# Performance work log

Measured on AMD Instinct MI355X. Metric: run time of the kernel, lower is better.

Reference implementation:

```python
import jax, jax.numpy as jnp
import numpy as np

N0 = 100000; E0 = 1600000; N1 = 100000; E1 = 1600000; G = 512
F0 = 93; F1 = 43
BN_EPS = 1e-5


def setup_inputs() -> dict:
    key = jax.random.key(0)
    ks = jax.random.split(key, 20)
    p = lambda i, shape: jax.random.normal(ks[i], shape, jnp.float32) * 0.02
    return {
        "x_0": jax.random.normal(ks[0], (N0, F0), jnp.float32),
        "x_1": jax.random.normal(ks[1], (N1, F1), jnp.float32),
        "edge_index_0": jax.random.randint(ks[2], (2, E0), 0, N0, jnp.int32),
        "edge_index_1": jax.random.randint(ks[3], (2, E1), 0, N1, jnp.int32),
        "batch_0": jnp.sort(jax.random.randint(ks[4], (N0,), 0, G, jnp.int32)),
        "batch_1": jnp.sort(jax.random.randint(ks[5], (N1,), 0, G, jnp.int32)),
        "w_c1": p(6, (F0, F0)), "b_c1": jnp.zeros((F0,), jnp.float32),
        "w_c2": p(7, (F0, F0 * 10)), "b_c2": jnp.zeros((F0 * 10,), jnp.float32),
        "w_c3": p(8, (F1, F1)), "b_c3": jnp.zeros((F1,), jnp.float32),
        "w_c4": p(9, (F1, F1 * 10)), "b_c4": jnp.zeros((F1 * 10,), jnp.float32),
        "g0_w1": p(10, (F0 * 10 * 2, 1024)), "g0_b1": jnp.zeros((1024,), jnp.float32),
        "g0_w2": p(11, (1024, 512)), "g0_b2": jnp.zeros((512,), jnp.float32),
        "g0_bn_g": jnp.ones((512,), jnp.float32), "g0_bn_b": jnp.zeros((512,), jnp.float32),
        "g1_w1": p(12, (F1 * 10 * 2, 1024)), "g1_b1": jnp.zeros((1024,), jnp.float32),
        "g1_w2": p(13, (1024, 512)), "g1_b2": jnp.zeros((512,), jnp.float32),
        "g1_bn_g": jnp.ones((512,), jnp.float32), "g1_bn_b": jnp.zeros((512,), jnp.float32),
        "f0_w1": p(14, (512, 256)), "f0_b1": jnp.zeros((256,), jnp.float32),
        "f0_w2": p(15, (256, 2)), "f0_b2": jnp.zeros((2,), jnp.float32),
        "f1_w1": p(16, (512, 256)), "f1_b1": jnp.zeros((256,), jnp.float32),
        "f1_w2": p(17, (256, 2)), "f1_b2": jnp.zeros((2,), jnp.float32),
    }


def gin_conv(x, edge_index, W, b):
    # GINConv(eps=0): nn(x + sum_{j->i} x_j); messages from src=edge_index[0] to dst=edge_index[1]
    agg = jax.ops.segment_sum(x[edge_index[0]], edge_index[1], num_segments=x.shape[0])
    return (x + agg) @ W + b


def pool_mean_max(x, batch):
    cnt = jax.ops.segment_sum(jnp.ones((x.shape[0], 1), x.dtype), batch, num_segments=G)
    mean = jax.ops.segment_sum(x, batch, num_segments=G) / jnp.maximum(cnt, 1.0)
    mx = jax.ops.segment_max(x, batch, num_segments=G)
    mx = jnp.where(cnt > 0, mx, 0.0)
    return jnp.concatenate([mean, mx], axis=1)


def batchnorm(x, g, b):
    m = x.mean(axis=0)
    v = x.var(axis=0)
    return g * (x - m) / jnp.sqrt(v + BN_EPS) + b


def branch(x, ei, batch, w_a, b_a, w_b, b_b, w1, b1, w2, b2, bn_g, bn_b):
    h = jax.nn.relu(gin_conv(x, ei, w_a, b_a))
    h = jax.nn.relu(gin_conv(h, ei, w_b, b_b))
    h = pool_mean_max(h, batch)              # [G, 2*10*F] ; PairNorm(mode='None') is identity
    h = jax.nn.relu(h @ w1 + b1)             # dropout: eval mode (identity)
    h = h @ w2 + b2
    return batchnorm(h, bn_g, bn_b)          # [G, 512]


def reference(x_0, x_1, edge_index_0, edge_index_1, batch_0, batch_1,
              w_c1, b_c1, w_c2, b_c2, w_c3, b_c3, w_c4, b_c4,
              g0_w1, g0_b1, g0_w2, g0_b2, g0_bn_g, g0_bn_b,
              g1_w1, g1_b1, g1_w2, g1_b2, g1_bn_g, g1_bn_b,
              f0_w1, f0_b1, f0_w2, f0_b2, f1_w1, f1_b1, f1_w2, f1_b2):
    x_g_0 = branch(x_0, edge_index_0, batch_0, w_c1, b_c1, w_c2, b_c2,
                   g0_w1, g0_b1, g0_w2, g0_b2, g0_bn_g, g0_bn_b)
    z = jax.nn.relu(x_g_0 @ f0_w1 + f0_b1) @ f0_w2 + f0_b2
    x_g_1 = branch(x_1, edge_index_1, batch_1, w_c3, b_c3, w_c4, b_c4,
                   g1_w1, g1_b1, g1_w2, g1_b2, g1_bn_g, g1_bn_b)
    z1 = jax.nn.relu(x_g_1 @ f1_w1 + f1_b1) @ f1_w2 + f1_b2
    return (z, x_g_0, x_g_1, z1)
```

## Files before the change

### kernel.cpp

```cpp
#include <hip/hip_runtime.h>
#include <hip/hip_bf16.h>

#define N0 100000
#define E0C 1600000
#define N1 100000
#define E1C 1600000
#define GCONST 512
#define F0C 93
#define F1C 43
#define OC0 (F0C * 10)
#define OC1 (F1C * 10)
#define BN_EPS 1e-5f
#define NBKT 391
#define SLAB 6016

typedef __attribute__((ext_vector_type(8))) short short8;
typedef __attribute__((ext_vector_type(4))) float floatx4;

static __device__ __forceinline__ unsigned short f2bf(float f) {
    unsigned u = __float_as_uint(f);
    unsigned r = (u + 0x7FFF + ((u >> 16) & 1)) >> 16;
    return (unsigned short)r;
}
static __device__ __forceinline__ float bf2f(unsigned short u) {
    return __uint_as_float(((unsigned)u) << 16);
}
static __device__ __forceinline__ void split_bf(float v, unsigned short& h, unsigned short& l) {
    h = f2bf(v);
    l = f2bf(v - bf2f(h));
}

__global__ __launch_bounds__(256) void misc_kernel(const int* __restrict__ bat0,
                                                   const int* __restrict__ bat1,
                                                   int* __restrict__ st0,
                                                   int* __restrict__ st1,
                                                   int* __restrict__ bcur2) {
    int bid = blockIdx.x;
    int t = threadIdx.x;
    if (bid < 6) {
        int branch = bid / 3;
        const int* batch = branch ? bat1 : bat0;
        int* starts = branch ? st1 : st0;
        int g = (bid % 3) * 256 + t;
        if (g > GCONST) return;
        if (g == GCONST) { starts[GCONST] = N0; return; }
        int lo = 0, hi = N0;
        while (lo < hi) {
            int mid = (lo + hi) >> 1;
            if (batch[mid] < g) lo = mid + 1; else hi = mid;
        }
        starts[g] = lo;
    } else {
        for (int i = t; i < 1024; i += 256) {
            if (i < NBKT) bcur2[i] = i * SLAB;
            else if (i >= 512 && i < 512 + NBKT) bcur2[i] = (i - 512) * SLAB;
        }
    }
}

__global__ __launch_bounds__(256) void edge_bucket2_kernel(const int* __restrict__ ei0,
                                                           const int* __restrict__ ei1,
                                                           int E, int* __restrict__ bcur2,
                                                           int2* __restrict__ st0,
                                                           int2* __restrict__ st1,
                                                           const float* __restrict__ Wc1,
                                                           const float* __restrict__ Wc2,
                                                           const float* __restrict__ Wc3,
                                                           const float* __restrict__ Wc4,
                                                           unsigned short* __restrict__ Ta0,
                                                           unsigned short* __restrict__ Tb0,
                                                           unsigned short* __restrict__ Ta1,
                                                           unsigned short* __restrict__ Tb1,
                                                           unsigned short* __restrict__ p0h,
                                                           unsigned short* __restrict__ p0l,
                                                           unsigned short* __restrict__ p1h,
                                                           unsigned short* __restrict__ p1l) {
    int bid = blockIdx.x;
    int t = threadIdx.x;
    if (bid < 1564) {
        int branch = bid >= 782;
        int blk = branch ? bid - 782 : bid;
        const int* ei = branch ? ei1 : ei0;
        int* bcur = bcur2 + branch * 512;
        int2* staging = branch ? st1 : st0;
        __shared__ int hist[NBKT];
        __shared__ int gbase[NBKT];
        for (int i = t; i < NBKT; i += 256) hist[i] = 0;
        __syncthreads();
        int base = blk * 2048;
        int srcv[8], dstv[8];
#pragma unroll
        for (int i = 0; i < 8; ++i) {
            int e = base + i * 256 + t;
            if (e < E) { srcv[i] = ei[e]; dstv[i] = ei[E + e]; }
            else dstv[i] = -1;
        }
#pragma unroll
        for (int i = 0; i < 8; ++i)
            if (dstv[i] >= 0) atomicAdd(&hist[dstv[i] >> 8], 1);
        __syncthreads();
        for (int i = t; i < NBKT; i += 256) {
            int c = hist[i];
            gbase[i] = c ? atomicAdd(&bcur[i], c) : 0;
            hist[i] = 0;
        }
        __syncthreads();
#pragma unroll
        for (int i = 0; i < 8; ++i) {
            if (dstv[i] >= 0) {
                int b = dstv[i] >> 8;
                int lofs = atomicAdd(&hist[b], 1);
                staging[gbase[b] + lofs] = make_int2(srcv[i], dstv[i]);
            }
        }
    } else if (bid < 3612) {
        int idx = bid - 1564;
        int cfg = idx >> 9;
        int c = (idx & 511) * 2 + (t >> 7);
        int k = t & 127;
        const float* W; unsigned short* T; int OCr, Fr, KP, RB;
        switch (cfg) {
            case 0:  W = Wc1; T = Ta0; OCr = 93;  Fr = 93; KP = 96; RB = 96;   break;
            case 1:  W = Wc2; T = Tb0; OCr = 930; Fr = 93; KP = 96; RB = 1024; break;
            case 2:  W = Wc3; T = Ta1; OCr = 43;  Fr = 43; KP = 64; RB = 48;   break;
            default: W = Wc4; T = Tb1; OCr = 430; Fr = 43; KP = 64; RB = 512;  break;
        }
        if (c >= RB || k >= KP) return;
        unsigned short v = 0;
        if (c < OCr && k < Fr) v = f2bf(W[(size_t)k * OCr + c]);
        T[(size_t)c * KP + k] = v;
    } else if (bid < 3732) {
        int i = (bid - 3612) * 256 + t;
        if (i >= GCONST * 60) return;
        int g = i / 60, c = 1860 + (i - g * 60);
        p0h[(size_t)g * 1920 + c] = 0;
        p0l[(size_t)g * 1920 + c] = 0;
    } else {
        int i = (bid - 3732) * 256 + t;
        if (i >= GCONST * 36) return;
        int g = i / 36, c = 860 + (i - g * 36);
        p1h[(size_t)g * 896 + c] = 0;
        p1l[(size_t)g * 896 + c] = 0;
    }
}

__global__ __launch_bounds__(512) void bucket_scan2_kernel(const int* __restrict__ bcur2,
                                                           int* __restrict__ bbase2) {
    const int* bcur = bcur2 + blockIdx.x * 512;
    int* bbase = bbase2 + blockIdx.x * 512;
    __shared__ int sh[512];
    int t = threadIdx.x;
    int cnt = (t < NBKT) ? bcur[t] - t * SLAB : 0;
    sh[t] = cnt;
    __syncthreads();
    for (int o = 1; o < 512; o <<= 1) {
        int add = (t >= o) ? sh[t - o] : 0;
        __syncthreads();
        sh[t] += add;
        __syncthreads();
    }
    if (t <= NBKT) bbase[t] = sh[t] - cnt;
}

static __device__ __forceinline__ void csr_build_dev(int b, const int2* __restrict__ staging,
                                                     const int* __restrict__ bcur,
                                                     const int* __restrict__ bbase, int N,
                                                     int* __restrict__ rowptr,
                                                     int* __restrict__ col) {
    __shared__ int h[256];
    __shared__ int sc[256];
    int t = threadIdx.x;
    int sl = b * SLAB;
    int se = bcur[b];
    int go = bbase[b];
    h[t] = 0;
    __syncthreads();
    for (int i = sl + t; i < se; i += 256)
        atomicAdd(&h[staging[i].y & 255], 1);
    __syncthreads();
    int v = h[t];
    sc[t] = v;
    __syncthreads();
    for (int o = 1; o < 256; o <<= 1) {
        int add = (t >= o) ? sc[t - o] : 0;
        __syncthreads();
        sc[t] += add;
        __syncthreads();
    }
    int ex = go + (sc[t] - v);
    int node = (b << 8) + t;
    if (node <= N) rowptr[node] = ex;
    __syncthreads();
    sc[t] = ex;
    __syncthreads();
    for (int i = sl + t; i < se; i += 256) {
        int2 ed = staging[i];
        int pos = atomicAdd(&sc[ed.y & 255], 1);
        col[pos] = ed.x;
    }
}

static __device__ __forceinline__ void wsplit_dev(int k0, int c0,
                                                  const float* __restrict__ W,
                                                  unsigned short* __restrict__ Th,
                                                  unsigned short* __restrict__ Tl,
                                                  int K, int N, int KP) {
    __shared__ float tile[32][33];
    int tx = threadIdx.x & 31, ty = threadIdx.x >> 5;
    for (int r = ty; r < 32; r += 8) {
        int k = k0 + r;
        tile[r][tx] = (k < K) ? W[(size_t)k * N + c0 + tx] : 0.f;
    }
    __syncthreads();
    for (int r = ty; r < 32; r += 8) {
        int c = c0 + r;
        float v = tile[tx][r];
        unsigned short h, l;
        split_bf(v, h, l);
        Th[(size_t)c * KP + k0 + tx] = h;
        Tl[(size_t)c * KP + k0 + tx] = l;
    }
}

template<int KP, int CH, int GR>
static __device__ __forceinline__ void gather_dev(int nb, unsigned short* __restrict__ t,
                                                  const unsigned short* __restrict__ x,
                                                  const int* __restrict__ rowptr,
                                                  const int* __restrict__ col, int N) {
    int wave = threadIdx.x >> 6, lane = threadIdx.x & 63;
    int node = nb * 4 + wave;
    if (node >= N) return;
    int g = lane / CH;
    int c = lane - g * CH;
    bool act = (g < GR);
    int s = rowptr[node], e = rowptr[node + 1];
    float acc[8] = {0.f, 0.f, 0.f, 0.f, 0.f, 0.f, 0.f, 0.f};
    int j = act ? (s - 1 + g) : e;
    int src0 = node;
    if (j >= s && j < e) src0 = col[j];
    while (j < e) {
        int jb = j + GR;
        int jc = jb + GR;
        int srcb = (jb < e) ? col[jb] : 0;
        int srcc = (jc < e) ? col[jc] : 0;
        short8 v0 = *(const short8*)(x + (size_t)src0 * KP + c * 8);
#pragma unroll
        for (int i = 0; i < 8; ++i) acc[i] += bf2f((unsigned short)v0[i]);
        if (jb < e) {
            short8 v1 = *(const short8*)(x + (size_t)srcb * KP + c * 8);
#pragma unroll
            for (int i = 0; i < 8; ++i) acc[i] += bf2f((unsigned short)v1[i]);
        }
        j = jc; src0 = srcc;
    }
    if (GR == 8) {
#pragma unroll
        for (int i = 0; i < 8; ++i) {
            float v = acc[i];
            v += __shfl_xor(v, 8);
            v += __shfl_xor(v, 16);
            v += __shfl_xor(v, 32);
            acc[i] = v;
        }
    } else {
#pragma unroll
        for (int i = 0; i < 8; ++i) {
            float v = acc[i];
            float v1 = __shfl(v, lane + CH);
            float v2 = __shfl(v, lane + 2 * CH);
            float v3 = __shfl(v, lane + 3 * CH);
            float v4 = __shfl(v, lane + 4 * CH);
            acc[i] = v + v1 + v2 + v3 + v4;
        }
    }
    if (lane < CH) {
        short8 o;
#pragma unroll
        for (int i = 0; i < 8; ++i) o[i] = (short)f2bf(acc[i]);
        *(short8*)(t + (size_t)node * KP + lane * 8) = o;
    }
}

template<int KP, int KS, int NT>
static __device__ __forceinline__ void conv1_dev(int nb, const unsigned short* __restrict__ t,
                                                 const unsigned short* __restrict__ Wt,
                                                 const float* __restrict__ bias,
                                                 unsigned short* __restrict__ y,
                                                 int NC, int N) {
    int wave = threadIdx.x >> 6, lane = threadIdx.x & 63;
    int quad = lane >> 4, l15 = lane & 15;
    int r0 = (nb * 4 + wave) * 16;
    const short8 z8 = {0, 0, 0, 0, 0, 0, 0, 0};
    short8 a[KS];
    int arow = r0 + l15;
#pragma unroll
    for (int ks = 0; ks < KS; ++ks)
        a[ks] = (arow < N) ? *(const short8*)(t + (size_t)arow * KP + ks * 32 + quad * 8) : z8;
#pragma unroll
    for (int nt = 0; nt < NT; ++nt) {
        int colb = nt * 16 + l15;
        floatx4 c = {0.f, 0.f, 0.f, 0.f};
#pragma unroll
        for (int ks = 0; ks < KS; ++ks) {
            short8 b = *(const short8*)(Wt + (size_t)colb * KP + ks * 32 + quad * 8);
            c = __builtin_amdgcn_mfma_f32_16x16x32_bf16(a[ks], b, c, 0, 0, 0);
        }
        float bc = (colb < NC) ? bias[colb] : 0.f;
#pragma unroll
        for (int r = 0; r < 4; ++r) {
            int row = r0 + quad * 4 + r;
            if (row < N) {
                float o = fmaxf(c[r] + bc, 0.f);
                y[(size_t)row * KP + colb] = f2bf(o);
            }
        }
    }
}

template<int KP, int KS>
static __device__ __forceinline__ void conv2_pool_dev(int cb, int g,
                                                      const unsigned short* __restrict__ t,
                                                      const unsigned short* __restrict__ Wt,
                                                      const float* __restrict__ bias,
                                                      const int* __restrict__ starts,
                                                      unsigned short* __restrict__ ph,
                                                      unsigned short* __restrict__ pl,
                                                      int OC, int KPad) {
    int wave = threadIdx.x >> 6, lane = threadIdx.x & 63;
    int quad = lane >> 4, l15 = lane & 15;
    int cw0 = cb * 256 + wave * 64;
    short8 bfr[4][KS];
    float bs[4];
#pragma unroll
    for (int ti = 0; ti < 4; ++ti) {
        int colb = cw0 + ti * 16 + l15;
#pragma unroll
        for (int ks = 0; ks < KS; ++ks)
            bfr[ti][ks] = *(const short8*)(Wt + (size_t)colb * KP + ks * 32 + quad * 8);
        bs[ti] = (colb < OC) ? bias[colb] : 0.f;
    }
    int s = starts[g], e = starts[g + 1];
    float sum[4] = {0.f, 0.f, 0.f, 0.f};
    float mx[4]  = {0.f, 0.f, 0.f, 0.f};
    const short8 z8 = {0, 0, 0, 0, 0, 0, 0, 0};
    for (int ns = s; ns < e; ns += 16) {
        short8 a[KS];
        int arow = ns + l15;
        bool av = arow < e;
#pragma unroll
        for (int ks = 0; ks < KS; ++ks)
            a[ks] = av ? *(const short8*)(t + (size_t)arow * KP + ks * 32 + quad * 8) : z8;
        int rbase = ns + quad * 4;
#pragma unroll
        for (int ti = 0; ti < 4; ++ti) {
            floatx4 c = {0.f, 0.f, 0.f, 0.f};
#pragma unroll
            for (int ks = 0; ks < KS; ++ks)
                c = __builtin_amdgcn_mfma_f32_16x16x32_bf16(a[ks], bfr[ti][ks], c, 0, 0, 0);
#pragma unroll
            for (int r = 0; r < 4; ++r) {
                float o = fmaxf(c[r] + bs[ti], 0.f);
                if (rbase + r < e) {
                    sum[ti] += o;
                    mx[ti] = fmaxf(mx[ti], o);
                }
            }
        }
    }
    int cnt = e - s;
    float rc = 1.f / (float)(cnt > 0 ? cnt : 1);
#pragma unroll
    for (int ti = 0; ti < 4; ++ti) {
        float sv = sum[ti], mv = mx[ti];
        sv += __shfl_down(sv, 32);
        mv = fmaxf(mv, __shfl_down(mv, 32));
        sv += __shfl_down(sv, 16);
        mv = fmaxf(mv, __shfl_down(mv, 16));
        if (lane < 16) {
            int colb = cw0 + ti * 16 + l15;
            if (colb < OC) {
                size_t base = (size_t)g * (size_t)KPad;
                unsigned short h, l;
                split_bf(sv * rc, h, l);
                ph[base + colb] = h; pl[base + colb] = l;
                split_bf(mv, h, l);
                ph[base + OC + colb] = h; pl[base + OC + colb] = l;
            }
        }
    }
}

template<int MODE>
static __device__ __forceinline__ void gemm3x_dev(int bx, int by, int NBX,
                                                  const unsigned short* __restrict__ Ah,
                                                  const unsigned short* __restrict__ Al,
                                                  const unsigned short* __restrict__ Bh,
                                                  const unsigned short* __restrict__ Bl,
                                                  const float* __restrict__ bias,
                                                  float* __restrict__ Cf,
                                                  unsigned short* __restrict__ Ch,
                                                  unsigned short* __restrict__ Cl,
                                                  int KP) {
    int wave = threadIdx.x >> 6, lane = threadIdx.x & 63;
    int quad = lane >> 4, l15 = lane & 15;
    int r0 = by * 32 + (wave & 1) * 16;
    int c0 = bx * 64 + (wave >> 1) * 32;
    int Ncols = NBX * 64;
    floatx4 acc0 = {0.f, 0.f, 0.f, 0.f};
    floatx4 acc1 = {0.f, 0.f, 0.f, 0.f};
    const unsigned short* arh = Ah + (size_t)(r0 + l15) * KP;
    const unsigned short* arl = Al + (size_t)(r0 + l15) * KP;
    const unsigned short* b0h = Bh + (size_t)(c0 + l15) * KP;
    const unsigned short* b0l = Bl + (size_t)(c0 + l15) * KP;
    const unsigned short* b1h = Bh + (size_t)(c0 + 16 + l15) * KP;
    const unsigned short* b1l = Bl + (size_t)(c0 + 16 + l15) * KP;
    for (int k0 = 0; k0 < KP; k0 += 128) {
        short8 ah[4], al[4];
#pragma unroll
        for (int q = 0; q < 4; ++q) {
            ah[q] = *(const short8*)(arh + k0 + q * 32 + quad * 8);
            al[q] = *(const short8*)(arl + k0 + q * 32 + quad * 8);
        }
#pragma unroll
        for (int q = 0; q < 4; ++q) {
            short8 bh = *(const short8*)(b0h + k0 + q * 32 + quad * 8);
            short8 bl = *(const short8*)(b0l + k0 + q * 32 + quad * 8);
            acc0 = __builtin_amdgcn_mfma_f32_16x16x32_bf16(ah[q], bh, acc0, 0, 0, 0);
            acc0 = __builtin_amdgcn_mfma_f32_16x16x32_bf16(al[q], bh, acc0, 0, 0, 0);
            acc0 = __builtin_amdgcn_mfma_f32_16x16x32_bf16(ah[q], bl, acc0, 0, 0, 0);
            bh = *(const short8*)(b1h + k0 + q * 32 + quad * 8);
            bl = *(const short8*)(b1l + k0 + q * 32 + quad * 8);
            acc1 = __builtin_amdgcn_mfma_f32_16x16x32_bf16(ah[q], bh, acc1, 0, 0, 0);
            acc1 = __builtin_amdgcn_mfma_f32_16x16x32_bf16(al[q], bh, acc1, 0, 0, 0);
            acc1 = __builtin_amdgcn_mfma_f32_16x16x32_bf16(ah[q], bl, acc1, 0, 0, 0);
        }
    }
    int col0 = c0 + l15, col1 = c0 + 16 + l15;
    float bc0 = bias[col0], bc1 = bias[col1];
#pragma unroll
    for (int r = 0; r < 4; ++r) {
        int row = r0 + quad * 4 + r;
        float v0 = acc0[r] + bc0;
        float v1 = acc1[r] + bc1;
        if (MODE != 1) { v0 = fmaxf(v0, 0.f); v1 = fmaxf(v1, 0.f); }
        if (MODE == 0) {
            unsigned short h, l;
            split_bf(v0, h, l);
            Ch[(size_t)row * Ncols + col0] = h; Cl[(size_t)row * Ncols + col0] = l;
            split_bf(v1, h, l);
            Ch[(size_t)row * Ncols + col1] = h; Cl[(size_t)row * Ncols + col1] = l;
        } else {
            Cf[(size_t)row * Ncols + col0] = v0;
            Cf[(size_t)row * Ncols + col1] = v1;
        }
    }
}

static __device__ __forceinline__ void bn_dev(int c, const float* __restrict__ p,
                                              const float* __restrict__ gamma,
                                              const float* __restrict__ beta,
                                              float* __restrict__ outp,
                                              unsigned short* __restrict__ oh,
                                              unsigned short* __restrict__ ol) {
    __shared__ float ls[256], ls2[256];
    int t = threadIdx.x;
    float v0 = p[(size_t)t * 512 + c];
    float v1 = p[(size_t)(t + 256) * 512 + c];
    ls[t] = v0 + v1;
    ls2[t] = v0 * v0 + v1 * v1;
    __syncthreads();
    for (int st = 128; st > 0; st >>= 1) {
        if (t < st) { ls[t] += ls[t + st]; ls2[t] += ls2[t + st]; }
        __syncthreads();
    }
    if (t == 0) {
        float m = ls[0] / 512.f;
        float var = ls2[0] / 512.f - m * m;
        ls[0] = m;
        ls2[0] = 1.f / sqrtf(var + BN_EPS);
    }
    __syncthreads();
    float m = ls[0], iv = ls2[0];
    float g = gamma[c], b = beta[c];
    float w0 = g * (v0 - m) * iv + b;
    float w1 = g * (v1 - m) * iv + b;
    outp[(size_t)t * 512 + c] = w0;
    outp[(size_t)(t + 256) * 512 + c] = w1;
    unsigned short h, l;
    split_bf(w0, h, l);
    oh[(size_t)t * 512 + c] = h; ol[(size_t)t * 512 + c] = l;
    split_bf(w1, h, l);
    oh[(size_t)(t + 256) * 512 + c] = h; ol[(size_t)(t + 256) * 512 + c] = l;
}

static __device__ __forceinline__ void head2_dev(int nb, const float* __restrict__ h,
                                                 const float* __restrict__ w2,
                                                 const float* __restrict__ b2,
                                                 float* __restrict__ z, int M) {
    int wave = threadIdx.x >> 6, lane = threadIdx.x & 63;
    int row = nb * 4 + wave;
    if (row >= M) return;
    float4 hv = *(const float4*)(h + (size_t)row * 256 + lane * 4);
    const float* wp = w2 + lane * 8;
    float s0 = hv.x * wp[0] + hv.y * wp[2] + hv.z * wp[4] + hv.w * wp[6];
    float s1 = hv.x * wp[1] + hv.y * wp[3] + hv.z * wp[5] + hv.w * wp[7];
#pragma unroll
    for (int offd = 32; offd >= 1; offd >>= 1) {
        s0 += __shfl_down(s0, offd);
        s1 += __shfl_down(s1, offd);
    }
    if (lane == 0) {
        z[(size_t)row * 2 + 0] = s0 + b2[0];
        z[(size_t)row * 2 + 1] = s1 + b2[1];
    }
}


__global__ __launch_bounds__(256) void f0_kernel(const int2* __restrict__ st0,
                                                 const int2* __restrict__ st1,
                                                 const int* __restrict__ bcur2,
                                                 const int* __restrict__ bbase2,
                                                 int* __restrict__ rp0, int* __restrict__ rp1,
                                                 int* __restrict__ c0, int* __restrict__ c1,
                                                 unsigned short* __restrict__ xb0,
                                                 const float* __restrict__ x0,
                                                 unsigned short* __restrict__ xb1,
                                                 const float* __restrict__ x1) {
    int bid = blockIdx.x;
    if (bid < 2 * NBKT) {
        int branch = bid >= NBKT;
        csr_build_dev(branch ? bid - NBKT : bid,
                      branch ? st1 : st0,
                      bcur2 + branch * 512, bbase2 + branch * 512, N0,
                      branch ? rp1 : rp0, branch ? c1 : c0);
    } else if (bid < 2 * NBKT + 50000) {
        int b = bid - 2 * NBKT;
        int node = b * 2 + (threadIdx.x >> 7);
        int f = threadIdx.x & 127;
        if (node < N0 && f < 96)
            xb0[(size_t)node * 96 + f] = (f < 93) ? f2bf(x0[(size_t)node * 93 + f]) : (unsigned short)0;
    } else {
        int b = bid - 2 * NBKT - 50000;
        int node = b * 4 + (threadIdx.x >> 6);
        int f = threadIdx.x & 63;
        if (node < N1)
            xb1[(size_t)node * 64 + f] = (f < 43) ? f2bf(x1[(size_t)node * 43 + f]) : (unsigned short)0;
    }
}

__global__ __launch_bounds__(256) void f1_kernel(unsigned short* __restrict__ tb,
                                                 const unsigned short* __restrict__ xb0,
                                                 const int* __restrict__ rowptr0,
                                                 const int* __restrict__ col0,
                                                 const float* g0_w1, const float* g0_w2,
                                                 const float* f0_w1,
                                                 const float* g1_w1, const float* g1_w2,
                                                 const float* f1_w1,
                                                 unsigned short* bt1h0, unsigned short* bt1l0,
                                                 unsigned short* bt2h0, unsigned short* bt2l0,
                                                 unsigned short* bt3h0, unsigned short* bt3l0,
                                                 unsigned short* bt1h1, unsigned short* bt1l1,
                                                 unsigned short* bt2h1, unsigned short* bt2l1,
                                                 unsigned short* bt3h1, unsigned short* bt3l1) {
    int bid = blockIdx.x;
    if (bid < 25000) {
        gather_dev<96, 12, 5>(bid, tb, xb0, rowptr0, col0, N0);
        return;
    }
    int w = bid - 25000;
    if (w < 1920)      wsplit_dev((w % 60) * 32, (w / 60) * 32, g0_w1, bt1h0, bt1l0, 1860, 1024, 1920);
    else if (w < 2432) { w -= 1920; wsplit_dev((w % 32) * 32, (w / 32) * 32, g0_w2, bt2h0, bt2l0, 1024, 512, 1024); }
    else if (w < 2560) { w -= 2432; wsplit_dev((w % 16) * 32, (w / 16) * 32, f0_w1, bt3h0, bt3l0, 512, 256, 512); }
    else if (w < 3456) { w -= 2560; wsplit_dev((w % 28) * 32, (w / 28) * 32, g1_w1, bt1h1, bt1l1, 860, 1024, 896); }
    else if (w < 3968) { w -= 3456; wsplit_dev((w % 32) * 32, (w / 32) * 32, g1_w2, bt2h1, bt2l1, 1024, 512, 1024); }
    else               { w -= 3968; wsplit_dev((w % 16) * 32, (w / 16) * 32, f1_w1, bt3h1, bt3l1, 512, 256, 512); }
}

__global__ __launch_bounds__(256) void f2_kernel(unsigned short* __restrict__ t1,
                                                 const unsigned short* __restrict__ xb1,
                                                 const int* __restrict__ rowptr1,
                                                 const int* __restrict__ col1,
                                                 const unsigned short* __restrict__ tb,
                                                 const unsigned short* __restrict__ wt_a0,
                                                 const float* __restrict__ b_c1,
                                                 unsigned short* __restrict__ yb) {
    int bid = blockIdx.x;
    if (bid < 25000)
        gather_dev<64, 8, 8>(bid, t1, xb1, rowptr1, col1, N1);
    else
        conv1_dev<96, 3, 6>(bid - 25000, tb, wt_a0, b_c1, yb, 93, N0);
}

__global__ __launch_bounds__(256) void f3_kernel(unsigned short* __restrict__ tb,
                                                 const unsigned short* __restrict__ yb,
                                                 const int* __restrict__ rowptr0,
                                                 const int* __restrict__ col0,
                                                 const unsigned short* __restrict__ t1,
                                                 const unsigned short* __restrict__ wt_a1,
                                                 const float* __restrict__ b_c3,
                                                 unsigned short* __restrict__ y1) {
    int bid = blockIdx.x;
    if (bid < 25000)
        gather_dev<96, 12, 5>(bid, tb, yb, rowptr0, col0, N0);
    else
        conv1_dev<64, 2, 3>(bid - 25000, t1, wt_a1, b_c3, y1, 43, N1);
}

__global__ __launch_bounds__(256) void f4_kernel(unsigned short* __restrict__ t1,
                                                 const unsigned short* __restrict__ y1,
                                                 const int* __restrict__ rowptr1,
                                                 const int* __restrict__ col1) {
    gather_dev<64, 8, 8>(blockIdx.x, t1, y1, rowptr1, col1, N1);
}

__global__ __launch_bounds__(256) void f5_kernel(const unsigned short* __restrict__ tb,
                                                 const unsigned short* __restrict__ wt_b0,
                                                 const float* __restrict__ b_c2,
                                                 const int* __restrict__ starts0,
                                                 unsigned short* __restrict__ p0h,
                                                 unsigned short* __restrict__ p0l,
                                                 const unsigned short* __restrict__ t1,
                                                 const unsigned short* __restrict__ wt_b1,
                                                 const float* __restrict__ b_c4,
                                                 const int* __restrict__ starts1,
                                                 unsigned short* __restrict__ p1h,
                                                 unsigned short* __restrict__ p1l) {
    int bid = blockIdx.x;
    if (bid < 2048) {
        int b = bid;
        int g = (b & 7) | ((b >> 5) << 3);
        int cb = (b >> 3) & 3;
        conv2_pool_dev<96, 3>(cb, g, tb, wt_b0, b_c2, starts0, p0h, p0l, OC0, 1920);
    } else {
        int b = bid - 2048;
        int g = (b & 7) | ((b >> 4) << 3);
        int cb = (b >> 3) & 1;
        conv2_pool_dev<64, 2>(cb, g, t1, wt_b1, b_c4, starts1, p1h, p1l, OC1, 896);
    }
}

__global__ __launch_bounds__(256) void f6_kernel(const unsigned short* __restrict__ p0h,
                                                 const unsigned short* __restrict__ p0l,
                                                 const unsigned short* __restrict__ bt1h0,
                                                 const unsigned short* __restrict__ bt1l0,
                                                 const float* __restrict__ g0_b1,
                                                 unsigned short* __restrict__ m1h0,
                                                 unsigned short* __restrict__ m1l0,
                                                 const unsigned short* __restrict__ p1h,
                                                 const unsigned short* __restrict__ p1l,
                                                 const unsigned short* __restrict__ bt1h1,
                                                 const unsigned short* __restrict__ bt1l1,
                                                 const float* __restrict__ g1_b1,
                                                 unsigned short* __restrict__ m1h1,
                                                 unsigned short* __restrict__ m1l1) {
    int bid = blockIdx.x;
    if (bid < 256)
        gemm3x_dev<0>(bid & 15, bid >> 4, 16, p0h, p0l, bt1h0, bt1l0, g0_b1,
                      nullptr, m1h0, m1l0, 1920);
    else {
        int b = bid - 256;
        gemm3x_dev<0>(b & 15, b >> 4, 16, p1h, p1l, bt1h1, bt1l1, g1_b1,
                      nullptr, m1h1, m1l1, 896);
    }
}

__global__ __launch_bounds__(256) void f7_kernel(const unsigned short* __restrict__ m1h0,
                                                 const unsigned short* __restrict__ m1l0,
                                                 const unsigned short* __restrict__ bt2h0,
                                                 const unsigned short* __restrict__ bt2l0,
                                                 const float* __restrict__ g0_b2,
                                                 float* __restrict__ pbn0,
                                                 const unsigned short* __restrict__ m1h1,
                                                 const unsigned short* __restrict__ m1l1,
                                                 const unsigned short* __restrict__ bt2h1,
                                                 const unsigned short* __restrict__ bt2l1,
                                                 const float* __restrict__ g1_b2,
                                                 float* __restrict__ pbn1) {
    int bid = blockIdx.x;
    if (bid < 128)
        gemm3x_dev<1>(bid & 7, bid >> 3, 8, m1h0, m1l0, bt2h0, bt2l0, g0_b2,
                      pbn0, nullptr, nullptr, 1024);
    else {
        int b = bid - 128;
        gemm3x_dev<1>(b & 7, b >> 3, 8, m1h1, m1l1, bt2h1, bt2l1, g1_b2,
                      pbn1, nullptr, nullptr, 1024);
    }
}

__global__ __launch_bounds__(256) void f8_kernel(const float* __restrict__ pbn0,
                                                 const float* __restrict__ g0_bn_g,
                                                 const float* __restrict__ g0_bn_b,
                                                 float* __restrict__ out_xg0,
                                                 unsigned short* __restrict__ xgh0,
                                                 unsigned short* __restrict__ xgl0,
                                                 const float* __restrict__ pbn1,
                                                 const float* __restrict__ g1_bn_g,
                                                 const float* __restrict__ g1_bn_b,
                                                 float* __restrict__ out_xg1,
                                                 unsigned short* __restrict__ xgh1,
                                                 unsigned short* __restrict__ xgl1) {
    int bid = blockIdx.x;
    if (bid < 512)
        bn_dev(bid, pbn0, g0_bn_g, g0_bn_b, out_xg0, xgh0, xgl0);
    else
        bn_dev(bid - 512, pbn1, g1_bn_g, g1_bn_b, out_xg1, xgh1, xgl1);
}

__global__ __launch_bounds__(256) void f9_kernel(const unsigned short* __restrict__ xgh0,
                                                 const unsigned short* __restrict__ xgl0,
                                                 const unsigned short* __restrict__ bt3h0,
                                                 const unsigned short* __restrict__ bt3l0,
                                                 const float* __restrict__ f0_b1,
                                                 float* __restrict__ hbuf0,
                                                 const unsigned short* __restrict__ xgh1,
                                                 const unsigned short* __restrict__ xgl1,
                                                 const unsigned short* __restrict__ bt3h1,
                                                 const unsigned short* __restrict__ bt3l1,
                                                 const float* __restrict__ f1_b1,
                                                 float* __restrict__ hbuf1) {
    int bid = blockIdx.x;
    if (bid < 64)
        gemm3x_dev<2>(bid & 3, bid >> 2, 4, xgh0, xgl0, bt3h0, bt3l0, f0_b1,
                      hbuf0, nullptr, nullptr, 512);
    else {
        int b = bid - 64;
        gemm3x_dev<2>(b & 3, b >> 2, 4, xgh1, xgl1, bt3h1, bt3l1, f1_b1,
                      hbuf1, nullptr, nullptr, 512);
    }
}

__global__ __launch_bounds__(256) void f10_kernel(const float* __restrict__ hbuf0,
                                                  const float* __restrict__ f0_w2,
                                                  const float* __restrict__ f0_b2,
                                                  float* __restrict__ out_z,
                                                  const float* __restrict__ hbuf1,
                                                  const float* __restrict__ f1_w2,
                                                  const float* __restrict__ f1_b2,
                                                  float* __restrict__ out_z1) {
    int bid = blockIdx.x;
    if (bid < 128)
        head2_dev(bid, hbuf0, f0_w2, f0_b2, out_z, GCONST);
    else
        head2_dev(bid - 128, hbuf1, f1_w2, f1_b2, out_z1, GCONST);
}

static inline int ceildiv(int a, int b) { return (a + b - 1) / b; }

extern "C" void kernel_launch(void* const* d_in, const int* in_sizes, int n_in,
                              void* d_out, int out_size, void* d_ws, size_t ws_size,
                              hipStream_t stream) {
    const float* x0   = (const float*)d_in[0];
    const float* x1   = (const float*)d_in[1];
    const int*   ei0  = (const int*)d_in[2];
    const int*   ei1  = (const int*)d_in[3];
    const int*   bat0 = (const int*)d_in[4];
    const int*   bat1 = (const int*)d_in[5];
    const float* w_c1 = (const float*)d_in[6];
    const float* b_c1 = (const float*)d_in[7];
    const float* w_c2 = (const float*)d_in[8];
    const float* b_c2 = (const float*)d_in[9];
    const float* w_c3 = (const float*)d_in[10];
    const float* b_c3 = (const float*)d_in[11];
    const float* w_c4 = (const float*)d_in[12];
    const float* b_c4 = (const float*)d_in[13];
    const float* g0_w1 = (const float*)d_in[14];
    const float* g0_b1 = (const float*)d_in[15];
    const float* g0_w2 = (const float*)d_in[16];
    const float* g0_b2 = (const float*)d_in[17];
    const float* g0_bn_g = (const float*)d_in[18];
    const float* g0_bn_b = (const float*)d_in[19];
    const float* g1_w1 = (const float*)d_in[20];
    const float* g1_b1 = (const float*)d_in[21];
    const float* g1_w2 = (const float*)d_in[22];
    const float* g1_b2 = (const float*)d_in[23];
    const float* g1_bn_g = (const float*)d_in[24];
    const float* g1_bn_b = (const float*)d_in[25];
    const float* f0_w1 = (const float*)d_in[26];
    const float* f0_b1 = (const float*)d_in[27];
    const float* f0_w2 = (const float*)d_in[28];
    const float* f0_b2 = (const float*)d_in[29];
    const float* f1_w1 = (const float*)d_in[30];
    const float* f1_b1 = (const float*)d_in[31];
    const float* f1_w2 = (const float*)d_in[32];
    const float* f1_b2 = (const float*)d_in[33];

    float* out = (float*)d_out;
    float* out_z   = out;
    float* out_xg0 = out + 1024;
    float* out_xg1 = out + 1024 + 262144;
    float* out_z1  = out + 1024 + 262144 + 262144;

    float* ws = (float*)d_ws;
    size_t off = 0;
    auto alloc = [&](size_t n) { float* p = ws + off; off += n; return p; };
    unsigned short* xb0 = (unsigned short*)alloc((size_t)N0 * 96 / 2);
    unsigned short* xb1 = (unsigned short*)alloc((size_t)N1 * 64 / 2);
    unsigned short* tb  = (unsigned short*)alloc((size_t)N0 * 96 / 2);
    unsigned short* yb  = (unsigned short*)alloc((size_t)N0 * 96 / 2);
    unsigned short* wt_a0 = (unsigned short*)alloc(96 * 96 / 2);
    unsigned short* wt_b0 = (unsigned short*)alloc(1024 * 96 / 2);
    unsigned short* wt_a1 = (unsigned short*)alloc(48 * 64 / 2);
    unsigned short* wt_b1 = (unsigned short*)alloc(512 * 64 / 2);
    unsigned short* bt1h0 = (unsigned short*)alloc((size_t)1024 * 1920 / 2);
    unsigned short* bt1l0 = (unsigned short*)alloc((size_t)1024 * 1920 / 2);
    unsigned short* bt2h0 = (unsigned short*)alloc((size_t)512 * 1024 / 2);
    unsigned short* bt2l0 = (unsigned short*)alloc((size_t)512 * 1024 / 2);
    unsigned short* bt3h0 = (unsigned short*)alloc((size_t)256 * 512 / 2);
    unsigned short* bt3l0 = (unsigned short*)alloc((size_t)256 * 512 / 2);
    unsigned short* bt1h1 = (unsigned short*)alloc((size_t)1024 * 896 / 2);
    unsigned short* bt1l1 = (unsigned short*)alloc((size_t)1024 * 896 / 2);
    unsigned short* bt2h1 = (unsigned short*)alloc((size_t)512 * 1024 / 2);
    unsigned short* bt2l1 = (unsigned short*)alloc((size_t)512 * 1024 / 2);
    unsigned short* bt3h1 = (unsigned short*)alloc((size_t)256 * 512 / 2);
    unsigned short* bt3l1 = (unsigned short*)alloc((size_t)256 * 512 / 2);
    unsigned short* m1h0 = (unsigned short*)alloc((size_t)512 * 1024 / 2);
    unsigned short* m1l0 = (unsigned short*)alloc((size_t)512 * 1024 / 2);
    unsigned short* m1h1 = (unsigned short*)alloc((size_t)512 * 1024 / 2);
    unsigned short* m1l1 = (unsigned short*)alloc((size_t)512 * 1024 / 2);
    unsigned short* xgh0 = (unsigned short*)alloc((size_t)512 * 512 / 2);
    unsigned short* xgl0 = (unsigned short*)alloc((size_t)512 * 512 / 2);
    unsigned short* xgh1 = (unsigned short*)alloc((size_t)512 * 512 / 2);
    unsigned short* xgl1 = (unsigned short*)alloc((size_t)512 * 512 / 2);
    unsigned short* p0h = (unsigned short*)alloc((size_t)512 * 1920 / 2);
    unsigned short* p0l = (unsigned short*)alloc((size_t)512 * 1920 / 2);
    unsigned short* p1h = (unsigned short*)alloc((size_t)512 * 896 / 2);
    unsigned short* p1l = (unsigned short*)alloc((size_t)512 * 896 / 2);
    float* pbn0  = alloc((size_t)512 * 512);
    float* pbn1  = alloc((size_t)512 * 512);
    float* hbuf0 = alloc((size_t)512 * 256);
    float* hbuf1 = alloc((size_t)512 * 256);
    int* bbase2 = (int*)alloc(1024);
    int* bcur2  = (int*)alloc(1024);
    int* rowptr0 = (int*)alloc(100016);
    int* col0    = (int*)alloc(E0C);
    int* rowptr1 = (int*)alloc(100016);
    int* col1    = (int*)alloc(E1C);
    int* starts0 = (int*)alloc(520);
    int* starts1 = (int*)alloc(520);
    int2* staging0 = (int2*)tb;
    int2* staging1 = (int2*)yb;
    unsigned short* t1 = xb0;
    unsigned short* y1 = xb1;

    misc_kernel<<<7, 256, 0, stream>>>(bat0, bat1, starts0, starts1, bcur2);
    edge_bucket2_kernel<<<3804, 256, 0, stream>>>(ei0, ei1, E0C, bcur2,
                                                  staging0, staging1,
                                                  w_c1, w_c2, w_c3, w_c4,
                                                  wt_a0, wt_b0, wt_a1, wt_b1,
                                                  p0h, p0l, p1h, p1l);
    bucket_scan2_kernel<<<2, 512, 0, stream>>>(bcur2, bbase2);
    f0_kernel<<<2 * NBKT + 50000 + 25000, 256, 0, stream>>>(
        staging0, staging1, bcur2, bbase2, rowptr0, rowptr1, col0, col1,
        xb0, x0, xb1, x1);

    f1_kernel<<<25000 + 4096, 256, 0, stream>>>(
        tb, xb0, rowptr0, col0,
        g0_w1, g0_w2, f0_w1, g1_w1, g1_w2, f1_w1,
        bt1h0, bt1l0, bt2h0, bt2l0, bt3h0, bt3l0,
        bt1h1, bt1l1, bt2h1, bt2l1, bt3h1, bt3l1);
    f2_kernel<<<25000 + 1563, 256, 0, stream>>>(t1, xb1, rowptr1, col1,
                                                tb, wt_a0, b_c1, yb);
    f3_kernel<<<25000 + 1563, 256, 0, stream>>>(tb, yb, rowptr0, col0,
                                                t1, wt_a1, b_c3, y1);
    f4_kernel<<<25000, 256, 0, stream>>>(t1, y1, rowptr1, col1);
    f5_kernel<<<2048 + 1024, 256, 0, stream>>>(tb, wt_b0, b_c2, starts0, p0h, p0l,
                                               t1, wt_b1, b_c4, starts1, p1h, p1l);
    f6_kernel<<<256 + 256, 256, 0, stream>>>(p0h, p0l, bt1h0, bt1l0, g0_b1, m1h0, m1l0,
                                             p1h, p1l, bt1h1, bt1l1, g1_b1, m1h1, m1l1);
    f7_kernel<<<128 + 128, 256, 0, stream>>>(m1h0, m1l0, bt2h0, bt2l0, g0_b2, pbn0,
                                             m1h1, m1l1, bt2h1, bt2l1, g1_b2, pbn1);
    f8_kernel<<<512 + 512, 256, 0, stream>>>(pbn0, g0_bn_g, g0_bn_b, out_xg0, xgh0, xgl0,
                                             pbn1, g1_bn_g, g1_bn_b, out_xg1, xgh1, xgl1);
    f9_kernel<<<64 + 64, 256, 0, stream>>>(xgh0, xgl0, bt3h0, bt3l0, f0_b1, hbuf0,
                                           xgh1, xgl1, bt3h1, bt3l1, f1_b1, hbuf1);
    f10_kernel<<<128 + 128, 256, 0, stream>>>(hbuf0, f0_w2, f0_b2, out_z,
                                              hbuf1, f1_w2, f1_b2, out_z1);
}
```

Before: 665.8 us.

## Split GIN neighbor gather into 32-feature column chunks across blocks

The neighbor-sum gather now splits each node's feature row into 32-element column chunks, each handled by a separate block. Within a wave, 16 edge groups times 4 lanes each read one 64-byte chunk, and the result is reduced with xor shuffles. This replaces the old layout where one wave covered the whole row with 5 or 8 edge groups. The aim is more edges in flight per wave and more parallelism per feature slice, better cache locality per chunk, and full use of all 64 lanes. In exchange it triples or doubles the block count and rereads rowptr/col once per chunk.

```diff
diff --git a/kernel.cpp b/kernel.cpp
--- a/kernel.cpp
+++ b/kernel.cpp
@@ -222,62 +222,50 @@
     }
 }
 
-template<int KP, int CH, int GR>
-static __device__ __forceinline__ void gather_dev(int nb, unsigned short* __restrict__ t,
-                                                  const unsigned short* __restrict__ x,
-                                                  const int* __restrict__ rowptr,
-                                                  const int* __restrict__ col, int N) {
+template<int KP>
+static __device__ __forceinline__ void gather_chunk_dev(int bid, int NB,
+                                                        unsigned short* __restrict__ t,
+                                                        const unsigned short* __restrict__ x,
+                                                        const int* __restrict__ rowptr,
+                                                        const int* __restrict__ col, int N) {
+    int chunk = bid / NB;
+    int nb = bid - chunk * NB;
     int wave = threadIdx.x >> 6, lane = threadIdx.x & 63;
     int node = nb * 4 + wave;
     if (node >= N) return;
-    int g = lane / CH;
-    int c = lane - g * CH;
-    bool act = (g < GR);
+    int g = lane >> 2;
+    int c = lane & 3;
+    int eoff = chunk * 32 + c * 8;
     int s = rowptr[node], e = rowptr[node + 1];
     float acc[8] = {0.f, 0.f, 0.f, 0.f, 0.f, 0.f, 0.f, 0.f};
-    int j = act ? (s - 1 + g) : e;
+    int j = s - 1 + g;
     int src0 = node;
     if (j >= s && j < e) src0 = col[j];
     while (j < e) {
-        int jb = j + GR;
-        int jc = jb + GR;
+        int jb = j + 16;
+        int jc = jb + 16;
         int srcb = (jb < e) ? col[jb] : 0;
         int srcc = (jc < e) ? col[jc] : 0;
-        short8 v0 = *(const short8*)(x + (size_t)src0 * KP + c * 8);
+        short8 v0 = *(const short8*)(x + (size_t)src0 * KP + eoff);
 #pragma unroll
         for (int i = 0; i < 8; ++i) acc[i] += bf2f((unsigned short)v0[i]);
         if (jb < e) {
-            short8 v1 = *(const short8*)(x + (size_t)srcb * KP + c * 8);
+            short8 v1 = *(const short8*)(x + (size_t)srcb * KP + eoff);
 #pragma unroll
             for (int i = 0; i < 8; ++i) acc[i] += bf2f((unsigned short)v1[i]);
         }
         j = jc; src0 = srcc;
     }
-    if (GR == 8) {
-#pragma unroll
-        for (int i = 0; i < 8; ++i) {
-            float v = acc[i];
-            v += __shfl_xor(v, 8);
-            v += __shfl_xor(v, 16);
-            v += __shfl_xor(v, 32);
-            acc[i] = v;
-        }
-    } else {
-#pragma unroll
-        for (int i = 0; i < 8; ++i) {
-            float v = acc[i];
-            float v1 = __shfl(v, lane + CH);
-            float v2 = __shfl(v, lane + 2 * CH);
-            float v3 = __shfl(v, lane + 3 * CH);
-            float v4 = __shfl(v, lane + 4 * CH);
-            acc[i] = v + v1 + v2 + v3 + v4;
-        }
-    }
-    if (lane < CH) {
-        short8 o;
-#pragma unroll
-        for (int i = 0; i < 8; ++i) o[i] = (short)f2bf(acc[i]);
-        *(short8*)(t + (size_t)node * KP + lane * 8) = o;
+#pragma unroll
+    for (int o = 4; o < 64; o <<= 1) {
+#pragma unroll
+        for (int i = 0; i < 8; ++i) acc[i] += __shfl_xor(acc[i], o);
+    }
+    if (lane < 4) {
+        short8 o8;
+#pragma unroll
+        for (int i = 0; i < 8; ++i) o8[i] = (short)f2bf(acc[i]);
+        *(short8*)(t + (size_t)node * KP + chunk * 32 + lane * 8) = o8;
     }
 }
 
@@ -563,11 +551,11 @@
                                                  unsigned short* bt2h1, unsigned short* bt2l1,
                                                  unsigned short* bt3h1, unsigned short* bt3l1) {
     int bid = blockIdx.x;
-    if (bid < 25000) {
-        gather_dev<96, 12, 5>(bid, tb, xb0, rowptr0, col0, N0);
+    if (bid < 75000) {
+        gather_chunk_dev<96>(bid, 25000, tb, xb0, rowptr0, col0, N0);
         return;
     }
-    int w = bid - 25000;
+    int w = bid - 75000;
     if (w < 1920)      wsplit_dev((w % 60) * 32, (w / 60) * 32, g0_w1, bt1h0, bt1l0, 1860, 1024, 1920);
     else if (w < 2432) { w -= 1920; wsplit_dev((w % 32) * 32, (w / 32) * 32, g0_w2, bt2h0, bt2l0, 1024, 512, 1024); }
     else if (w < 2560) { w -= 2432; wsplit_dev((w % 16) * 32, (w / 16) * 32, f0_w1, bt3h0, bt3l0, 512, 256, 512); }
@@ -585,10 +573,10 @@
                                                  const float* __restrict__ b_c1,
                                                  unsigned short* __restrict__ yb) {
     int bid = blockIdx.x;
-    if (bid < 25000)
-        gather_dev<64, 8, 8>(bid, t1, xb1, rowptr1, col1, N1);
+    if (bid < 50000)
+        gather_chunk_dev<64>(bid, 25000, t1, xb1, rowptr1, col1, N1);
     else
-        conv1_dev<96, 3, 6>(bid - 25000, tb, wt_a0, b_c1, yb, 93, N0);
+        conv1_dev<96, 3, 6>(bid - 50000, tb, wt_a0, b_c1, yb, 93, N0);
 }
 
 __global__ __launch_bounds__(256) void f3_kernel(unsigned short* __restrict__ tb,
@@ -600,17 +588,17 @@
                                                  const float* __restrict__ b_c3,
                                                  unsigned short* __restrict__ y1) {
     int bid = blockIdx.x;
-    if (bid < 25000)
-        gather_dev<96, 12, 5>(bid, tb, yb, rowptr0, col0, N0);
+    if (bid < 75000)
+        gather_chunk_dev<96>(bid, 25000, tb, yb, rowptr0, col0, N0);
     else
-        conv1_dev<64, 2, 3>(bid - 25000, t1, wt_a1, b_c3, y1, 43, N1);
+        conv1_dev<64, 2, 3>(bid - 75000, t1, wt_a1, b_c3, y1, 43, N1);
 }
 
 __global__ __launch_bounds__(256) void f4_kernel(unsigned short* __restrict__ t1,
                                                  const unsigned short* __restrict__ y1,
                                                  const int* __restrict__ rowptr1,
                                                  const int* __restrict__ col1) {
-    gather_dev<64, 8, 8>(blockIdx.x, t1, y1, rowptr1, col1, N1);
+    gather_chunk_dev<64>(blockIdx.x, 25000, t1, y1, rowptr1, col1, N1);
 }
 
 __global__ __launch_bounds__(256) void f5_kernel(const unsigned short* __restrict__ tb,
@@ -853,16 +841,16 @@
         staging0, staging1, bcur2, bbase2, rowptr0, rowptr1, col0, col1,
         xb0, x0, xb1, x1);
 
-    f1_kernel<<<25000 + 4096, 256, 0, stream>>>(
+    f1_kernel<<<75000 + 4096, 256, 0, stream>>>(
         tb, xb0, rowptr0, col0,
         g0_w1, g0_w2, f0_w1, g1_w1, g1_w2, f1_w1,
         bt1h0, bt1l0, bt2h0, bt2l0, bt3h0, bt3l0,
         bt1h1, bt1l1, bt2h1, bt2l1, bt3h1, bt3l1);
-    f2_kernel<<<25000 + 1563, 256, 0, stream>>>(t1, xb1, rowptr1, col1,
+    f2_kernel<<<50000 + 1563, 256, 0, stream>>>(t1, xb1, rowptr1, col1,
                                                 tb, wt_a0, b_c1, yb);
-    f3_kernel<<<25000 + 1563, 256, 0, stream>>>(tb, yb, rowptr0, col0,
+    f3_kernel<<<75000 + 1563, 256, 0, stream>>>(tb, yb, rowptr0, col0,
                                                 t1, wt_a1, b_c3, y1);
-    f4_kernel<<<25000, 256, 0, stream>>>(t1, y1, rowptr1, col1);
+    f4_kernel<<<50000, 256, 0, stream>>>(t1, y1, rowptr1, col1);
     f5_kernel<<<2048 + 1024, 256, 0, stream>>>(tb, wt_b0, b_c2, starts0, p0h, p0l,
                                                t1, wt_b1, b_c4, starts1, p1h, p1l);
     f6_kernel<<<256 + 256, 256, 0, stream>>>(p0h, p0l, bt1h0, bt1l0, g0_b1, m1h0, m1l0,
```

After: 806.7 us. 21.2% more time.
